# Performance work log

Hardware: AMD Instinct MI355X
Metric: run time of the kernel (lower is better)

## Reference

```python
import jax, jax.numpy as jnp
import numpy as np

EPS = 1e-5

def _ln(x, g, b):
    # layer norm over last dim
    m = jnp.mean(x, axis=-1, keepdims=True)
    v = jnp.mean((x - m) ** 2, axis=-1, keepdims=True)
    return (x - m) * jax.lax.rsqrt(v + EPS) * g + b

def setup_inputs() -> dict:
    key = jax.random.key(0)
    ks = jax.random.split(key, 12)
    B, T, E, H, OUT = 128, 256, 64, 128, 1
    GENOME = 1_000_000
    D = 2 * E  # input_size_lstm
    inp = {}
    inp["indices"] = jax.random.randint(ks[0], (B, T, 2), 0, GENOME, dtype=jnp.int64)
    inp["h0"] = jax.random.normal(ks[1], (B, H), dtype=jnp.float32)
    inp["c0"] = jax.random.normal(ks[2], (B, H), dtype=jnp.float32)
    inp["embed_table"] = jax.random.normal(ks[3], (GENOME, E), dtype=jnp.float32)
    s_ih = 1.0 / np.sqrt(D)
    s_hh = 1.0 / np.sqrt(H)
    inp["W_ih"] = jax.random.uniform(ks[4], (4 * H, D), minval=-s_ih, maxval=s_ih, dtype=jnp.float32)
    inp["W_hh"] = jax.random.uniform(ks[5], (4 * H, H), minval=-s_hh, maxval=s_hh, dtype=jnp.float32)
    inp["g_ih"] = jnp.ones((4 * H,), jnp.float32)
    inp["b_ih"] = jnp.zeros((4 * H,), jnp.float32)
    inp["g_hh"] = jnp.ones((4 * H,), jnp.float32)
    inp["b_hh"] = jnp.zeros((4 * H,), jnp.float32)
    inp["g_c"] = jnp.ones((H,), jnp.float32)
    inp["b_c"] = jnp.zeros((H,), jnp.float32)
    s_o = 1.0 / np.sqrt(H * T)
    inp["W_out"] = jax.random.uniform(ks[6], (OUT * T, H * T), minval=-s_o, maxval=s_o, dtype=jnp.float32)
    inp["b_out"] = jax.random.uniform(ks[7], (OUT * T,), minval=-s_o, maxval=s_o, dtype=jnp.float32)
    return inp

def _forward(indices, embed_table, W_ih, W_hh, g_ih, b_ih, g_hh, b_hh, g_c, b_c, W_out, b_out, h0, c0):
    B, T = indices.shape[0], indices.shape[1]
    H = h0.shape[-1]
    # embedding gather: (B,T,2,E) -> (B,T,2E)
    emb = embed_table[indices].reshape(B, T, -1)
    # precompute input-to-hidden gates for all timesteps: (B,T,4H)
    x_gates = jnp.einsum("btd,gd->btg", emb, W_ih)

    def step(carry, xg):
        h, c = carry
        gates = _ln(xg, g_ih, b_ih) + _ln(h @ W_hh.T, g_hh, b_hh)
        i, f, g, o = jnp.split(gates, 4, axis=-1)
        c_new = jax.nn.sigmoid(f) * c + jax.nn.sigmoid(i) * jnp.tanh(g)
        h_new = jax.nn.sigmoid(o) * jnp.tanh(_ln(c_new, g_c, b_c))
        return (h_new, c_new), h_new

    (_, _), hs = jax.lax.scan(step, (h0, c0), jnp.swapaxes(x_gates, 0, 1))
    # hs: (T,B,H) -> (B,T*H)
    seq_out = jnp.swapaxes(hs, 0, 1).reshape(B, T * H)
    out = jax.nn.sigmoid(seq_out @ W_out.T + b_out)
    return out, emb

def reference(indices, h0, c0, embed_table, W_ih, W_hh, g_ih, b_ih, g_hh, b_hh, g_c, b_c, W_out, b_out):
    return _forward(indices, embed_table, W_ih, W_hh, g_ih, b_ih, g_hh, b_hh, g_c, b_c, W_out, b_out, h0, c0)
```

## Files before the change

kernel.cpp:

```cpp
#include <hip/hip_runtime.h>
#include <cstddef>


__device__ __forceinline__ float frcp(float x) { return __builtin_amdgcn_rcpf(x); }
__device__ __forceinline__ float sigm(float x) { return frcp(1.0f + __expf(-x)); }
__device__ __forceinline__ float ftanh(float x) {
  float e = __expf(2.0f * x);
  return (e - 1.0f) * frcp(e + 1.0f);
}

__global__ void k_embed(const int* __restrict__ idx, const float4* __restrict__ table4,
                        float4* __restrict__ emb4) {
  int i = blockIdx.x * blockDim.x + threadIdx.x;
  int p = i >> 4, j = i & 15;
  int id = idx[p];
  emb4[(size_t)p * 16 + j] = table4[(size_t)id * 16 + j];
}

__global__ void k_transpose(const float* __restrict__ W, float* __restrict__ Wt) {
  int i = blockIdx.x * 256 + threadIdx.x;
  int g = i >> 7, k = i & 127;
  Wt[k * 512 + g] = W[i];
}

__global__ __launch_bounds__(256) void k_gemm_tn(
    const float* __restrict__ A, const float* __restrict__ Bm, float* __restrict__ C,
    int K, int kchunks, int N, size_t partstride)
{
  __shared__ float As[64][65];
  __shared__ float Bs[64][68];
  const int tid = threadIdx.x;
  const int tx = tid & 15, ty = tid >> 4;
  const int m0 = blockIdx.x * 64, n0 = blockIdx.y * 64;
  float acc[4][4] = {};
  size_t kbase = (size_t)blockIdx.z * kchunks * 64;
  for (int kc = 0; kc < kchunks; ++kc) {
    size_t k0 = kbase + (size_t)kc * 64;
    #pragma unroll
    for (int it = 0; it < 4; ++it) {
      int fi = it * 256 + tid;
      int row = fi >> 4, col4 = fi & 15;
      float4 va = *(const float4*)(A + (size_t)(m0 + row) * K + k0 + col4 * 4);
      As[row][col4*4+0] = va.x; As[row][col4*4+1] = va.y;
      As[row][col4*4+2] = va.z; As[row][col4*4+3] = va.w;
      float4 vb = *(const float4*)(Bm + (size_t)(n0 + row) * K + k0 + col4 * 4);
      Bs[col4*4+0][row] = vb.x; Bs[col4*4+1][row] = vb.y;
      Bs[col4*4+2][row] = vb.z; Bs[col4*4+3][row] = vb.w;
    }
    __syncthreads();
    #pragma unroll 8
    for (int k = 0; k < 64; ++k) {
      float a0 = As[ty*4+0][k], a1 = As[ty*4+1][k], a2 = As[ty*4+2][k], a3 = As[ty*4+3][k];
      float b0 = Bs[k][tx*4+0], b1 = Bs[k][tx*4+1], b2 = Bs[k][tx*4+2], b3 = Bs[k][tx*4+3];
      acc[0][0] += a0*b0; acc[0][1] += a0*b1; acc[0][2] += a0*b2; acc[0][3] += a0*b3;
      acc[1][0] += a1*b0; acc[1][1] += a1*b1; acc[1][2] += a1*b2; acc[1][3] += a1*b3;
      acc[2][0] += a2*b0; acc[2][1] += a2*b1; acc[2][2] += a2*b2; acc[2][3] += a2*b3;
      acc[3][0] += a3*b0; acc[3][1] += a3*b1; acc[3][2] += a3*b2; acc[3][3] += a3*b3;
    }
    __syncthreads();
  }
  float* Cp = C + (size_t)blockIdx.z * partstride;
  #pragma unroll
  for (int i = 0; i < 4; ++i) {
    float4 v = make_float4(acc[i][0], acc[i][1], acc[i][2], acc[i][3]);
    *(float4*)(Cp + (size_t)(m0 + ty*4 + i) * N + n0 + tx*4) = v;
  }
}

__global__ __launch_bounds__(256) void k_xstats(const float4* __restrict__ xg4,
                                                float* __restrict__ xm, float* __restrict__ xr) {
  int row = blockIdx.x * 4 + (threadIdx.x >> 6);
  int lane = threadIdx.x & 63;
  const float4* r = xg4 + (size_t)row * 128;
  float4 a = r[lane], b = r[lane + 64];
  float s = a.x + a.y + a.z + a.w + b.x + b.y + b.z + b.w;
  float q = a.x*a.x + a.y*a.y + a.z*a.z + a.w*a.w + b.x*b.x + b.y*b.y + b.z*b.z + b.w*b.w;
  #pragma unroll
  for (int off = 32; off; off >>= 1) { s += __shfl_xor(s, off); q += __shfl_xor(q, off); }
  if (lane == 0) {
    float m = s * (1.0f / 512.0f);
    xm[row] = m;
    xr[row] = rsqrtf(q * (1.0f / 512.0f) - m * m + 1e-5f);
  }
}

__global__ __launch_bounds__(512, 2) void k_scan(
    const float* __restrict__ xg,
    const float* __restrict__ Wt,
    const float* __restrict__ xm, const float* __restrict__ xr,
    const float* __restrict__ h0, const float* __restrict__ c0,
    const float* __restrict__ g_ih, const float* __restrict__ b_ih,
    const float* __restrict__ g_hh, const float* __restrict__ b_hh,
    const float* __restrict__ g_c,  const float* __restrict__ b_c,
    float* __restrict__ hs)
{
  const int b = blockIdx.x;
  const int g = threadIdx.x;
  const int lane = g & 63, wave = g >> 6;

  __shared__ float xv_s[2][512];
  __shared__ float acc_s[2][512];
  __shared__ float2 red_s[2][8];
  __shared__ float4 h4_s[8][32];

  float4 w4[32];
  #pragma unroll
  for (int k = 0; k < 32; ++k) {
    w4[k].x = Wt[(4*k+0) * 512 + g];
    w4[k].y = Wt[(4*k+1) * 512 + g];
    w4[k].z = Wt[(4*k+2) * 512 + g];
    w4[k].w = Wt[(4*k+3) * 512 + g];
  }
  #pragma unroll
  for (int k = 0; k < 32; ++k)
    asm volatile("" : "+v"(w4[k].x), "+v"(w4[k].y), "+v"(w4[k].z), "+v"(w4[k].w));

  float gih[8], bih[8], ghh[8], bhh[8];
  #pragma unroll
  for (int j = 0; j < 8; ++j) {
    gih[j] = g_ih[j*64 + lane]; bih[j] = b_ih[j*64 + lane];
    ghh[j] = g_hh[j*64 + lane]; bhh[j] = b_hh[j*64 + lane];
  }
  float gc0 = g_c[lane], bc0 = b_c[lane], gc1 = g_c[64 + lane], bc1 = b_c[64 + lane];
  float cv0 = c0[b*128 + lane], cv1 = c0[b*128 + 64 + lane];

  float* hown = (float*)&h4_s[wave][0];
  hown[lane]      = h0[b*128 + lane];
  hown[64 + lane] = h0[b*128 + 64 + lane];

  const float* xgb = xg + (size_t)b * 256 * 512;
  const float* xmb = xm + b * 256;
  const float* xrb = xr + b * 256;
  float* hsb = hs + (size_t)b * 256 * 128;

  for (int t = 0; t < 256; ++t) {
    const int buf = t & 1;
    float xv = xgb[t*512 + g];
    xv_s[buf][g] = xv;
    float mx = xmb[t], rx = xrb[t];

    float a0 = 0.f, a1 = 0.f, a2 = 0.f, a3 = 0.f;
    #pragma unroll
    for (int k = 0; k < 32; ++k) {
      float4 h4 = h4_s[wave][k];
      a0 += w4[k].x * h4.x; a1 += w4[k].y * h4.y;
      a2 += w4[k].z * h4.z; a3 += w4[k].w * h4.w;
    }
    float acc = (a0 + a1) + (a2 + a3);
    acc_s[buf][g] = acc;

    float s = acc, q = acc * acc;
    #pragma unroll
    for (int off = 32; off; off >>= 1) { s += __shfl_xor(s, off); q += __shfl_xor(q, off); }
    if (lane == 0) red_s[buf][wave] = make_float2(s, q);

    __syncthreads();

    float rsx = 0.f, rsq = 0.f;
    #pragma unroll
    for (int i = 0; i < 8; ++i) { float2 v = red_s[buf][i]; rsx += v.x; rsq += v.y; }
    float mh = rsx * (1.0f/512.0f), vh = rsq * (1.0f/512.0f) - mh * mh;
    float rh = rsqrtf(vh + 1e-5f);

    float gv[8];
    #pragma unroll
    for (int j = 0; j < 8; ++j) {
      int p = j*64 + lane;
      float lx = (xv_s[buf][p]  - mx) * rx * gih[j] + bih[j];
      float lh = (acc_s[buf][p] - mh) * rh * ghh[j] + bhh[j];
      gv[j] = lx + lh;
    }
    float cn0 = sigm(gv[2]) * cv0 + sigm(gv[0]) * ftanh(gv[4]);
    float cn1 = sigm(gv[3]) * cv1 + sigm(gv[1]) * ftanh(gv[5]);
    cv0 = cn0; cv1 = cn1;

    float cs = cn0 + cn1, cq = cn0*cn0 + cn1*cn1;
    #pragma unroll
    for (int off = 32; off; off >>= 1) { cs += __shfl_xor(cs, off); cq += __shfl_xor(cq, off); }
    float mc = cs * (1.0f/128.0f), vc = cq * (1.0f/128.0f) - mc * mc;
    float rc = rsqrtf(vc + 1e-5f);

    float hn0 = sigm(gv[6]) * ftanh((cn0 - mc) * rc * gc0 + bc0);
    float hn1 = sigm(gv[7]) * ftanh((cn1 - mc) * rc * gc1 + bc1);
    hown[lane]      = hn0;
    hown[64 + lane] = hn1;
    if (wave == 0) { hsb[t*128 + lane] = hn0; hsb[t*128 + 64 + lane] = hn1; }
  }
}

__global__ void k_reduce(const float* __restrict__ part, const float* __restrict__ b_out,
                         float* __restrict__ out) {
  int i = blockIdx.x * 256 + threadIdx.x;
  float s = b_out[i & 255];
  #pragma unroll
  for (int z = 0; z < 32; ++z) s += part[(size_t)z * 32768 + i];
  out[i] = sigm(s);
}

extern "C" void kernel_launch(void* const* d_in, const int* in_sizes, int n_in,
                              void* d_out, int out_size, void* d_ws, size_t ws_size,
                              hipStream_t stream) {
  const int*   idx   = (const int*)  d_in[0];
  const float* h0    = (const float*)d_in[1];
  const float* c0    = (const float*)d_in[2];
  const float* table = (const float*)d_in[3];
  const float* W_ih  = (const float*)d_in[4];
  const float* W_hh  = (const float*)d_in[5];
  const float* g_ih  = (const float*)d_in[6];
  const float* b_ih  = (const float*)d_in[7];
  const float* g_hh  = (const float*)d_in[8];
  const float* b_hh  = (const float*)d_in[9];
  const float* g_c   = (const float*)d_in[10];
  const float* b_c   = (const float*)d_in[11];
  const float* W_out = (const float*)d_in[12];
  const float* b_out = (const float*)d_in[13];

  float* out  = (float*)d_out;
  float* emb  = out + 32768;
  float* ws   = (float*)d_ws;
  float* xg   = ws;
  float* hsb  = ws + 16777216;
  float* wt   = ws + 20971520;
  float* part = ws + 21037056;
  float* xmv  = part;
  float* xrv  = part + 32768;

  k_embed<<<4096, 256, 0, stream>>>(idx, (const float4*)table, (float4*)emb);
  k_transpose<<<256, 256, 0, stream>>>(W_hh, wt);
  k_gemm_tn<<<dim3(512, 8, 1), 256, 0, stream>>>(emb, W_ih, xg, 128, 2, 512, 0);
  k_xstats<<<8192, 256, 0, stream>>>((const float4*)xg, xmv, xrv);
  k_scan<<<128, 512, 0, stream>>>(xg, wt, xmv, xrv, h0, c0, g_ih, b_ih, g_hh, b_hh, g_c, b_c, hsb);
  k_gemm_tn<<<dim3(2, 4, 32), 256, 0, stream>>>(hsb, W_out, part, 32768, 16, 256, 32768);
  k_reduce<<<128, 256, 0, stream>>>(part, b_out, out);
}
```

Measured before the change: 611.9 us.

## Use split-fp16 MFMA for recurrent matvec and pre-normalize input gates

```diff
diff --git a/kernel.cpp b/kernel.cpp
--- a/kernel.cpp
+++ b/kernel.cpp
@@ -1,6 +1,9 @@
 #include <hip/hip_runtime.h>
 #include <cstddef>
 
+
+typedef __attribute__((ext_vector_type(8))) _Float16 f16x8;
+typedef __attribute__((ext_vector_type(4))) float f32x4;
 
 __device__ __forceinline__ float frcp(float x) { return __builtin_amdgcn_rcpf(x); }
 __device__ __forceinline__ float sigm(float x) { return frcp(1.0f + __expf(-x)); }
@@ -8,6 +11,17 @@
   float e = __expf(2.0f * x);
   return (e - 1.0f) * frcp(e + 1.0f);
 }
+__device__ __forceinline__ void split2(float x, unsigned short& hi, unsigned short& lo) {
+  _Float16 h = (_Float16)x;
+  _Float16 l = (_Float16)((x - (float)h) * 2048.0f);
+  hi = *(unsigned short*)&h;
+  lo = *(unsigned short*)&l;
+}
+__device__ __forceinline__ void barrier_lds() {
+  asm volatile("s_waitcnt lgkmcnt(0)\n\ts_barrier" ::: "memory");
+}
+
+#define SEL4(v, jj) ((jj) == 0 ? (v)[0] : (jj) == 1 ? (v)[1] : (jj) == 2 ? (v)[2] : (v)[3])
 
 __global__ void k_embed(const int* __restrict__ idx, const float4* __restrict__ table4,
                         float4* __restrict__ emb4) {
@@ -15,12 +29,6 @@
   int p = i >> 4, j = i & 15;
   int id = idx[p];
   emb4[(size_t)p * 16 + j] = table4[(size_t)id * 16 + j];
-}
-
-__global__ void k_transpose(const float* __restrict__ W, float* __restrict__ Wt) {
-  int i = blockIdx.x * 256 + threadIdx.x;
-  int g = i >> 7, k = i & 127;
-  Wt[k * 512 + g] = W[i];
 }
 
 __global__ __launch_bounds__(256) void k_gemm_tn(
@@ -67,124 +75,198 @@
   }
 }
 
-__global__ __launch_bounds__(256) void k_xstats(const float4* __restrict__ xg4,
-                                                float* __restrict__ xm, float* __restrict__ xr) {
+__global__ __launch_bounds__(256) void k_xln(float4* __restrict__ xg4,
+                                             const float4* __restrict__ g4,
+                                             const float4* __restrict__ bi4,
+                                             const float4* __restrict__ bh4) {
   int row = blockIdx.x * 4 + (threadIdx.x >> 6);
   int lane = threadIdx.x & 63;
-  const float4* r = xg4 + (size_t)row * 128;
+  float4* r = xg4 + (size_t)row * 128;
   float4 a = r[lane], b = r[lane + 64];
   float s = a.x + a.y + a.z + a.w + b.x + b.y + b.z + b.w;
   float q = a.x*a.x + a.y*a.y + a.z*a.z + a.w*a.w + b.x*b.x + b.y*b.y + b.z*b.z + b.w*b.w;
   #pragma unroll
   for (int off = 32; off; off >>= 1) { s += __shfl_xor(s, off); q += __shfl_xor(q, off); }
-  if (lane == 0) {
-    float m = s * (1.0f / 512.0f);
-    xm[row] = m;
-    xr[row] = rsqrtf(q * (1.0f / 512.0f) - m * m + 1e-5f);
-  }
+  float m = s * (1.0f / 512.0f);
+  float rs = rsqrtf(q * (1.0f / 512.0f) - m * m + 1e-5f);
+  float4 ga = g4[lane], gb = g4[64 + lane];
+  float4 ia = bi4[lane], ib = bi4[64 + lane];
+  float4 ha = bh4[lane], hb = bh4[64 + lane];
+  a.x = (a.x - m) * rs * ga.x + ia.x + ha.x; a.y = (a.y - m) * rs * ga.y + ia.y + ha.y;
+  a.z = (a.z - m) * rs * ga.z + ia.z + ha.z; a.w = (a.w - m) * rs * ga.w + ia.w + ha.w;
+  b.x = (b.x - m) * rs * gb.x + ib.x + hb.x; b.y = (b.y - m) * rs * gb.y + ib.y + hb.y;
+  b.z = (b.z - m) * rs * gb.z + ib.z + hb.z; b.w = (b.w - m) * rs * gb.w + ib.w + hb.w;
+  r[lane] = a; r[lane + 64] = b;
+}
+
+__global__ void k_wprep(const float* __restrict__ Whh, uint4* __restrict__ wfh,
+                        uint4* __restrict__ wfl) {
+  int i = blockIdx.x * 256 + threadIdx.x;
+  int l = i & 63, kc = (i >> 6) & 3, mt = i >> 8;
+  int row = mt * 16 + (l & 15);
+  int kb = kc * 32 + 8 * (l >> 4);
+  float4 a = *(const float4*)(Whh + row * 128 + kb);
+  float4 c = *(const float4*)(Whh + row * 128 + kb + 4);
+  unsigned short h0,h1,h2,h3,h4,h5,h6,h7, l0,l1,l2,l3,l4,l5,l6,l7;
+  split2(a.x,h0,l0); split2(a.y,h1,l1); split2(a.z,h2,l2); split2(a.w,h3,l3);
+  split2(c.x,h4,l4); split2(c.y,h5,l5); split2(c.z,h6,l6); split2(c.w,h7,l7);
+  uint4 oh, ol;
+  oh.x = h0 | ((unsigned)h1 << 16); oh.y = h2 | ((unsigned)h3 << 16);
+  oh.z = h4 | ((unsigned)h5 << 16); oh.w = h6 | ((unsigned)h7 << 16);
+  ol.x = l0 | ((unsigned)l1 << 16); ol.y = l2 | ((unsigned)l3 << 16);
+  ol.z = l4 | ((unsigned)l5 << 16); ol.w = l6 | ((unsigned)l7 << 16);
+  wfh[i] = oh; wfl[i] = ol;
 }
 
 __global__ __launch_bounds__(512, 2) void k_scan(
-    const float* __restrict__ xg,
-    const float* __restrict__ Wt,
-    const float* __restrict__ xm, const float* __restrict__ xr,
+    const float* __restrict__ xln,
+    const uint4* __restrict__ wfh,
+    const uint4* __restrict__ wfl,
     const float* __restrict__ h0, const float* __restrict__ c0,
-    const float* __restrict__ g_ih, const float* __restrict__ b_ih,
-    const float* __restrict__ g_hh, const float* __restrict__ b_hh,
+    const float* __restrict__ g_hh,
     const float* __restrict__ g_c,  const float* __restrict__ b_c,
     float* __restrict__ hs)
 {
   const int b = blockIdx.x;
-  const int g = threadIdx.x;
-  const int lane = g & 63, wave = g >> 6;
-
-  __shared__ float xv_s[2][512];
-  __shared__ float acc_s[2][512];
-  __shared__ float2 red_s[2][8];
-  __shared__ float4 h4_s[8][32];
-
-  float4 w4[32];
-  #pragma unroll
-  for (int k = 0; k < 32; ++k) {
-    w4[k].x = Wt[(4*k+0) * 512 + g];
-    w4[k].y = Wt[(4*k+1) * 512 + g];
-    w4[k].z = Wt[(4*k+2) * 512 + g];
-    w4[k].w = Wt[(4*k+3) * 512 + g];
-  }
-  #pragma unroll
-  for (int k = 0; k < 32; ++k)
-    asm volatile("" : "+v"(w4[k].x), "+v"(w4[k].y), "+v"(w4[k].z), "+v"(w4[k].w));
-
-  float gih[8], bih[8], ghh[8], bhh[8];
-  #pragma unroll
-  for (int j = 0; j < 8; ++j) {
-    gih[j] = g_ih[j*64 + lane]; bih[j] = b_ih[j*64 + lane];
-    ghh[j] = g_hh[j*64 + lane]; bhh[j] = b_hh[j*64 + lane];
-  }
-  float gc0 = g_c[lane], bc0 = b_c[lane], gc1 = g_c[64 + lane], bc1 = b_c[64 + lane];
-  float cv0 = c0[b*128 + lane], cv1 = c0[b*128 + 64 + lane];
-
-  float* hown = (float*)&h4_s[wave][0];
-  hown[lane]      = h0[b*128 + lane];
-  hown[64 + lane] = h0[b*128 + 64 + lane];
-
-  const float* xgb = xg + (size_t)b * 256 * 512;
-  const float* xmb = xm + b * 256;
-  const float* xrb = xr + b * 256;
+  const int tid = threadIdx.x;
+  const int w = tid >> 6, l = tid & 63;
+  const int lg = l >> 4;
+  const int jj = (l & 15) >> 2;
+  const bool wr = (l & 3) == 0;
+  const int u = w * 16 + lg * 4 + jj;
+  const float inv2048 = 1.0f / 2048.0f;
+
+  __shared__ alignas(16) unsigned short hbh[128];
+  __shared__ alignas(16) unsigned short hbl[128];
+  __shared__ float2 hred[8];
+  __shared__ float2 cred[8];
+
+  uint4 afh0[4], afh1[4], afh2[4], afh3[4];
+  uint4 afl0[4], afl1[4], afl2[4], afl3[4];
+  #pragma unroll
+  for (int kc = 0; kc < 4; ++kc) {
+    afh0[kc] = wfh[((w     ) * 4 + kc) * 64 + l];
+    afh1[kc] = wfh[((w +  8) * 4 + kc) * 64 + l];
+    afh2[kc] = wfh[((w + 16) * 4 + kc) * 64 + l];
+    afh3[kc] = wfh[((w + 24) * 4 + kc) * 64 + l];
+    afl0[kc] = wfl[((w     ) * 4 + kc) * 64 + l];
+    afl1[kc] = wfl[((w +  8) * 4 + kc) * 64 + l];
+    afl2[kc] = wfl[((w + 16) * 4 + kc) * 64 + l];
+    afl3[kc] = wfl[((w + 24) * 4 + kc) * 64 + l];
+  }
+  #pragma unroll
+  for (int kc = 0; kc < 4; ++kc) {
+    asm volatile("" : "+v"(afh0[kc].x), "+v"(afh0[kc].y), "+v"(afh0[kc].z), "+v"(afh0[kc].w));
+    asm volatile("" : "+v"(afh1[kc].x), "+v"(afh1[kc].y), "+v"(afh1[kc].z), "+v"(afh1[kc].w));
+    asm volatile("" : "+v"(afh2[kc].x), "+v"(afh2[kc].y), "+v"(afh2[kc].z), "+v"(afh2[kc].w));
+    asm volatile("" : "+v"(afh3[kc].x), "+v"(afh3[kc].y), "+v"(afh3[kc].z), "+v"(afh3[kc].w));
+    asm volatile("" : "+v"(afl0[kc].x), "+v"(afl0[kc].y), "+v"(afl0[kc].z), "+v"(afl0[kc].w));
+    asm volatile("" : "+v"(afl1[kc].x), "+v"(afl1[kc].y), "+v"(afl1[kc].z), "+v"(afl1[kc].w));
+    asm volatile("" : "+v"(afl2[kc].x), "+v"(afl2[kc].y), "+v"(afl2[kc].z), "+v"(afl2[kc].w));
+    asm volatile("" : "+v"(afl3[kc].x), "+v"(afl3[kc].y), "+v"(afl3[kc].z), "+v"(afl3[kc].w));
+  }
+
+  const float ghI = g_hh[u], ghF = g_hh[128 + u], ghG = g_hh[256 + u], ghO = g_hh[384 + u];
+  const float gcv = g_c[u], bcv = b_c[u];
+  float cv = c0[b * 128 + u];
+  if (wr) {
+    unsigned short hi, lo;
+    split2(h0[b * 128 + u], hi, lo);
+    hbh[u] = hi; hbl[u] = lo;
+  }
+  __syncthreads();
+
+  const float* xgb = xln + (size_t)b * 256 * 512;
   float* hsb = hs + (size_t)b * 256 * 128;
 
+  float xI = xgb[u], xF = xgb[128 + u], xG = xgb[256 + u], xO = xgb[384 + u];
+
   for (int t = 0; t < 256; ++t) {
-    const int buf = t & 1;
-    float xv = xgb[t*512 + g];
-    xv_s[buf][g] = xv;
-    float mx = xmb[t], rx = xrb[t];
-
-    float a0 = 0.f, a1 = 0.f, a2 = 0.f, a3 = 0.f;
-    #pragma unroll
-    for (int k = 0; k < 32; ++k) {
-      float4 h4 = h4_s[wave][k];
-      a0 += w4[k].x * h4.x; a1 += w4[k].y * h4.y;
-      a2 += w4[k].z * h4.z; a3 += w4[k].w * h4.w;
-    }
-    float acc = (a0 + a1) + (a2 + a3);
-    acc_s[buf][g] = acc;
-
-    float s = acc, q = acc * acc;
-    #pragma unroll
-    for (int off = 32; off; off >>= 1) { s += __shfl_xor(s, off); q += __shfl_xor(q, off); }
-    if (lane == 0) red_s[buf][wave] = make_float2(s, q);
-
-    __syncthreads();
+    const float* xn = xgb + (((t + 1) & 255) << 9);
+    float nI = xn[u], nF = xn[128 + u], nG = xn[256 + u], nO = xn[384 + u];
+
+    f32x4 acc0 = {0,0,0,0}, acc1 = {0,0,0,0}, acc2 = {0,0,0,0}, acc3 = {0,0,0,0};
+    f32x4 e0 = {0,0,0,0}, e1 = {0,0,0,0}, e2 = {0,0,0,0}, e3 = {0,0,0,0};
+    #pragma unroll
+    for (int kc = 0; kc < 4; ++kc) {
+      uint4 buh = *(const uint4*)((const char*)hbh + kc * 64 + 16 * lg);
+      uint4 bul = *(const uint4*)((const char*)hbl + kc * 64 + 16 * lg);
+      f16x8 bh = *(f16x8*)&buh;
+      f16x8 bl = *(f16x8*)&bul;
+      acc0 = __builtin_amdgcn_mfma_f32_16x16x32_f16(*(f16x8*)&afh0[kc], bh, acc0, 0, 0, 0);
+      acc1 = __builtin_amdgcn_mfma_f32_16x16x32_f16(*(f16x8*)&afh1[kc], bh, acc1, 0, 0, 0);
+      acc2 = __builtin_amdgcn_mfma_f32_16x16x32_f16(*(f16x8*)&afh2[kc], bh, acc2, 0, 0, 0);
+      acc3 = __builtin_amdgcn_mfma_f32_16x16x32_f16(*(f16x8*)&afh3[kc], bh, acc3, 0, 0, 0);
+      e0 = __builtin_amdgcn_mfma_f32_16x16x32_f16(*(f16x8*)&afh0[kc], bl, e0, 0, 0, 0);
+      e1 = __builtin_amdgcn_mfma_f32_16x16x32_f16(*(f16x8*)&afh1[kc], bl, e1, 0, 0, 0);
+      e2 = __builtin_amdgcn_mfma_f32_16x16x32_f16(*(f16x8*)&afh2[kc], bl, e2, 0, 0, 0);
+      e3 = __builtin_amdgcn_mfma_f32_16x16x32_f16(*(f16x8*)&afh3[kc], bl, e3, 0, 0, 0);
+      e0 = __builtin_amdgcn_mfma_f32_16x16x32_f16(*(f16x8*)&afl0[kc], bh, e0, 0, 0, 0);
+      e1 = __builtin_amdgcn_mfma_f32_16x16x32_f16(*(f16x8*)&afl1[kc], bh, e1, 0, 0, 0);
+      e2 = __builtin_amdgcn_mfma_f32_16x16x32_f16(*(f16x8*)&afl2[kc], bh, e2, 0, 0, 0);
+      e3 = __builtin_amdgcn_mfma_f32_16x16x32_f16(*(f16x8*)&afl3[kc], bh, e3, 0, 0, 0);
+    }
+    f32x4 a0, a1, a2, a3;
+    #pragma unroll
+    for (int j = 0; j < 4; ++j) {
+      a0[j] = acc0[j] + e0[j] * inv2048;
+      a1[j] = acc1[j] + e1[j] * inv2048;
+      a2[j] = acc2[j] + e2[j] * inv2048;
+      a3[j] = acc3[j] + e3[j] * inv2048;
+    }
+
+    float s = 0.f, q = 0.f;
+    #pragma unroll
+    for (int j = 0; j < 4; ++j) {
+      s += a0[j] + a1[j] + a2[j] + a3[j];
+      q += a0[j]*a0[j] + a1[j]*a1[j] + a2[j]*a2[j] + a3[j]*a3[j];
+    }
+    s += __shfl_xor(s, 16); s += __shfl_xor(s, 32);
+    q += __shfl_xor(q, 16); q += __shfl_xor(q, 32);
+    if (l == 0) hred[w] = make_float2(s, q);
+
+    barrier_lds();
 
     float rsx = 0.f, rsq = 0.f;
     #pragma unroll
-    for (int i = 0; i < 8; ++i) { float2 v = red_s[buf][i]; rsx += v.x; rsq += v.y; }
-    float mh = rsx * (1.0f/512.0f), vh = rsq * (1.0f/512.0f) - mh * mh;
-    float rh = rsqrtf(vh + 1e-5f);
-
-    float gv[8];
-    #pragma unroll
-    for (int j = 0; j < 8; ++j) {
-      int p = j*64 + lane;
-      float lx = (xv_s[buf][p]  - mx) * rx * gih[j] + bih[j];
-      float lh = (acc_s[buf][p] - mh) * rh * ghh[j] + bhh[j];
-      gv[j] = lx + lh;
-    }
-    float cn0 = sigm(gv[2]) * cv0 + sigm(gv[0]) * ftanh(gv[4]);
-    float cn1 = sigm(gv[3]) * cv1 + sigm(gv[1]) * ftanh(gv[5]);
-    cv0 = cn0; cv1 = cn1;
-
-    float cs = cn0 + cn1, cq = cn0*cn0 + cn1*cn1;
+    for (int i = 0; i < 8; ++i) { float2 v = hred[i]; rsx += v.x; rsq += v.y; }
+    float mh = rsx * (1.0f / 512.0f);
+    float rh = rsqrtf(rsq * (1.0f / 512.0f) - mh * mh + 1e-5f);
+
+    float aI = SEL4(a0, jj), aF = SEL4(a1, jj), aG = SEL4(a2, jj), aO = SEL4(a3, jj);
+    float gI = xI + (aI - mh) * rh * ghI;
+    float gF = xF + (aF - mh) * rh * ghF;
+    float gG = xG + (aG - mh) * rh * ghG;
+    float gO = xO + (aO - mh) * rh * ghO;
+
+    float cn = sigm(gF) * cv + sigm(gI) * ftanh(gG);
+    cv = cn;
+
+    float cs = cn, cq = cn * cn;
     #pragma unroll
     for (int off = 32; off; off >>= 1) { cs += __shfl_xor(cs, off); cq += __shfl_xor(cq, off); }
-    float mc = cs * (1.0f/128.0f), vc = cq * (1.0f/128.0f) - mc * mc;
-    float rc = rsqrtf(vc + 1e-5f);
-
-    float hn0 = sigm(gv[6]) * ftanh((cn0 - mc) * rc * gc0 + bc0);
-    float hn1 = sigm(gv[7]) * ftanh((cn1 - mc) * rc * gc1 + bc1);
-    hown[lane]      = hn0;
-    hown[64 + lane] = hn1;
-    if (wave == 0) { hsb[t*128 + lane] = hn0; hsb[t*128 + 64 + lane] = hn1; }
+    if (l == 0) cred[w] = make_float2(cs, cq);
+
+    barrier_lds();
+
+    float tcs = 0.f, tcq = 0.f;
+    #pragma unroll
+    for (int i = 0; i < 8; ++i) { float2 v = cred[i]; tcs += v.x; tcq += v.y; }
+    float mc = tcs * (1.0f / 512.0f);
+    float rc = rsqrtf(tcq * (1.0f / 512.0f) - mc * mc + 1e-5f);
+
+    float lnc = (cn - mc) * rc * gcv + bcv;
+    float hn = sigm(gO) * ftanh(lnc);
+
+    if (wr) {
+      unsigned short hi, lo;
+      split2(hn, hi, lo);
+      hbh[u] = hi; hbl[u] = lo;
+      hsb[(size_t)t * 128 + u] = hn;
+    }
+    xI = nI; xF = nF; xG = nG; xO = nO;
+
+    barrier_lds();
   }
 }
 
@@ -220,16 +302,16 @@
   float* ws   = (float*)d_ws;
   float* xg   = ws;
   float* hsb  = ws + 16777216;
-  float* wt   = ws + 20971520;
+  uint4* wfh  = (uint4*)(ws + 20971520);
+  uint4* wfl  = (uint4*)(ws + 21004288);
   float* part = ws + 21037056;
-  float* xmv  = part;
-  float* xrv  = part + 32768;
 
   k_embed<<<4096, 256, 0, stream>>>(idx, (const float4*)table, (float4*)emb);
-  k_transpose<<<256, 256, 0, stream>>>(W_hh, wt);
   k_gemm_tn<<<dim3(512, 8, 1), 256, 0, stream>>>(emb, W_ih, xg, 128, 2, 512, 0);
-  k_xstats<<<8192, 256, 0, stream>>>((const float4*)xg, xmv, xrv);
-  k_scan<<<128, 512, 0, stream>>>(xg, wt, xmv, xrv, h0, c0, g_ih, b_ih, g_hh, b_hh, g_c, b_c, hsb);
+  k_xln<<<8192, 256, 0, stream>>>((float4*)xg, (const float4*)g_ih,
+                                  (const float4*)b_ih, (const float4*)b_hh);
+  k_wprep<<<32, 256, 0, stream>>>(W_hh, wfh, wfl);
+  k_scan<<<128, 512, 0, stream>>>(xg, wfh, wfl, h0, c0, g_hh, g_c, b_c, hsb);
   k_gemm_tn<<<dim3(2, 4, 32), 256, 0, stream>>>(hsb, W_out, part, 32768, 16, 256, 32768);
   k_reduce<<<128, 256, 0, stream>>>(part, b_out, out);
 }
```

After: 649.4 us. +6.1%, slower.
